# Kernel optimization log

Measured on AMD Instinct MI355X. Metric: run time of the kernel, lower is better.

The kernel has to match this reference:

```python
import jax, jax.numpy as jnp
import numpy as np

CLS_NUM = 2
SCALE = 8.0
NO_OBJ_SCALE = 1.0
EPS = 1e-7


def setup_inputs() -> dict:
    key = jax.random.key(0)
    k1, k2, k3, k4, k5, k6 = jax.random.split(key, 6)
    B, C, H, W, N = 8, CLS_NUM, 512, 512, 160
    predict = jax.random.normal(k1, (B, C, H, W), dtype=jnp.float32)
    b = jax.random.randint(k2, (N,), 0, B).astype(jnp.float32)
    c = jax.random.randint(k3, (N,), 0, C).astype(jnp.float32)
    cxy = jax.random.uniform(k4, (N, 2), minval=0.0, maxval=H * SCALE)
    wh = jax.random.uniform(k5, (N, 2), minval=64.0, maxval=256.0)
    ang = jax.random.uniform(k6, (N, 1), minval=-np.pi, maxval=np.pi)
    targets = jnp.concatenate([b[:, None], c[:, None], cxy, wh, ang], axis=1).astype(jnp.float32)
    return {"predict": predict, "targets": targets}


def _forward(predict, targets):
    B, C, H, W = predict.shape
    pred = jnp.transpose(predict, (0, 2, 3, 1))          # [B,H,W,C]
    conf_all = jax.nn.sigmoid(pred)
    heatmap = jnp.max(conf_all, axis=-1)                 # [B,H,W]

    bid = targets[:, 0].astype(jnp.int32)                # [N] batch ids
    cid = targets[:, 1].astype(jnp.int32)                # [N] class ids
    cx = targets[:, 2] / SCALE
    cy = targets[:, 3] / SCALE
    w = targets[:, 4] / SCALE
    h = targets[:, 5] / SCALE
    ang = targets[:, 6]
    cos, sin = jnp.cos(ang), jnp.sin(ang)
    # rotate box center into the rotated frame (same math as render_map)
    x = cx * cos + cy * sin
    y = -cx * sin + cy * cos
    x3, x4 = x - h / 2, x + h / 2
    y3, y4 = y - w / 2, y + w / 2
    x1, x2 = x3 - 0.5, x4 + 0.5
    y1, y2 = y3 - 0.5, y4 + 0.5

    gx = jnp.arange(W, dtype=jnp.float32)[None, :] + 0.5  # [1,W] -> broadcasts to [H,W]
    gy = jnp.arange(H, dtype=jnp.float32)[:, None] + 0.5  # [H,1]
    vx = cos[:, None, None] * gx + sin[:, None, None] * gy   # [N,H,W]
    vy = -sin[:, None, None] * gx + cos[:, None, None] * gy  # [N,H,W]

    def box_mask(lo_x, hi_x, lo_y, hi_y):
        return ((lo_x[:, None, None] <= vx) & (vx <= hi_x[:, None, None]) &
                (lo_y[:, None, None] <= vy) & (vy <= hi_y[:, None, None]))

    inner = box_mask(x3, x4, y3, y4)  # obj region, [N,H,W]
    outer = box_mask(x1, x2, y1, y2)  # expanded region (clears noobj)

    loss = jnp.float32(0.0)
    for cls in range(CLS_NUM):
        sel = (cid == cls)[:, None, None]
        obj_cnt = jax.ops.segment_sum((inner & sel).astype(jnp.float32), bid, num_segments=B)
        out_cnt = jax.ops.segment_sum((outer & sel).astype(jnp.float32), bid, num_segments=B)
        obj_mask = obj_cnt > 0            # [B,H,W]
        noobj_mask = out_cnt <= 0         # starts at 1, zeroed inside any expanded box
        conf_c = jnp.clip(conf_all[..., cls], EPS, 1.0 - EPS)
        n_obj = jnp.sum(obj_mask)
        n_noobj = jnp.sum(noobj_mask)
        # BCE with target 1 on obj cells, target 0 on noobj cells (tconf == obj mask)
        loss_obj = -jnp.sum(jnp.where(obj_mask, jnp.log(conf_c), 0.0)) / jnp.maximum(n_obj, 1)
        loss_noobj = -jnp.sum(jnp.where(noobj_mask, jnp.log(1.0 - conf_c), 0.0)) / jnp.maximum(n_noobj, 1)
        loss = loss + jnp.where(n_obj > 0, loss_obj + NO_OBJ_SCALE * loss_noobj, 0.0)
    return loss, heatmap


def reference(predict, targets):
    return _forward(predict, targets)
```

## Files before the change

kernel.cpp:

```cpp
#include <hip/hip_runtime.h>
#include <math.h>

#define CLS 2
#define BATCH 8
#define HH 512
#define WW 512
#define EPSV 1e-7f
#define INV_SCALE 0.125f

#define TCAP 256
#define NB 512


__global__ __launch_bounds__(256) void heatmap_main(
    const float* __restrict__ predict, const float* __restrict__ targets,
    int nT, float* __restrict__ out, double* __restrict__ gsum,
    int* __restrict__ gcnt)
{
    __shared__ int s_cnt;
    __shared__ float s_cos[TCAP], s_sin[TCAP];
    __shared__ float s_x3[TCAP], s_x4[TCAP], s_y3[TCAP], s_y4[TCAP];
    __shared__ int   s_cid[TCAP];

    const int tid = threadIdx.x;
    const int blockPix = blockIdx.x * 256;
    const int b  = blockPix >> 18;
    const int i  = (blockPix >> 9) & (HH - 1);
    const int j0 = blockPix & (WW - 1);

    if (tid == 0) s_cnt = 0;
    __syncthreads();

    const float gy = (float)i + 0.5f;

    for (int t = tid; t < nT; t += 256) {
        const float* tp = targets + t * 7;
        const int tb = (int)tp[0];
        if (tb != b) continue;
        const float cx = tp[2] * INV_SCALE, cy = tp[3] * INV_SCALE;
        const float w_ = tp[4] * INV_SCALE, h_ = tp[5] * INV_SCALE;
        const float ang = tp[6];
        const float cs = cosf(ang), sn = sinf(ang);
        const float x = cx * cs + cy * sn;
        const float y = -cx * sn + cy * cs;
        const float x3 = x - 0.5f * h_, x4 = x + 0.5f * h_;
        const float y3 = y - 0.5f * w_, y4 = y + 0.5f * w_;

        const float gxl = (float)j0 + 0.5f, gxh = (float)j0 + 255.5f;
        const float a1 = cs * gxl + sn * gy, a2 = cs * gxh + sn * gy;
        const float vxlo = fminf(a1, a2), vxhi = fmaxf(a1, a2);
        const float b1 = -sn * gxl + cs * gy, b2 = -sn * gxh + cs * gy;
        const float vylo = fminf(b1, b2), vyhi = fmaxf(b1, b2);

        const float M = 0.51f;
        if (vxhi >= x3 - M && vxlo <= x4 + M && vyhi >= y3 - M && vylo <= y4 + M) {
            int slot = atomicAdd(&s_cnt, 1);
            s_cos[slot] = cs; s_sin[slot] = sn;
            s_x3[slot] = x3; s_x4[slot] = x4;
            s_y3[slot] = y3; s_y4[slot] = y4;
            s_cid[slot] = (int)tp[1];
        }
    }
    __syncthreads();
    const int cnt = s_cnt;

    const int j = j0 + tid;
    const float gx = (float)j + 0.5f;
    int objm = 0, outm = 0;
    for (int n = 0; n < cnt; ++n) {
        const float cs = s_cos[n], sn = s_sin[n];
        const float vx = cs * gx + sn * gy;
        const float vy = -sn * gx + cs * gy;
        const float x3 = s_x3[n], x4 = s_x4[n], y3 = s_y3[n], y4 = s_y4[n];
        const bool in_  = (x3 <= vx) & (vx <= x4) & (y3 <= vy) & (vy <= y4);
        const bool out_ = (x3 - 0.5f <= vx) & (vx <= x4 + 0.5f) &
                          (y3 - 0.5f <= vy) & (vy <= y4 + 0.5f);
        const int c = s_cid[n];
        objm |= ((int)in_) << c;
        outm |= ((int)out_) << c;
    }

    const int base = (b * CLS * HH + i) * WW + j;
    const float p0 = predict[base];
    const float p1 = predict[base + HH * WW];
    const float conf0 = __builtin_amdgcn_rcpf(1.0f + __expf(-p0));
    const float conf1 = __builtin_amdgcn_rcpf(1.0f + __expf(-p1));
    out[1 + (b * HH + i) * WW + j] = fmaxf(conf0, conf1);

    float so0 = 0.f, so1 = 0.f, sn0 = 0.f, sn1 = 0.f;
    int co0 = 0, co1 = 0, cn0 = 0, cn1 = 0;
    {
        const float cc0 = fminf(fmaxf(conf0, EPSV), 1.0f - EPSV);
        const float cc1 = fminf(fmaxf(conf1, EPSV), 1.0f - EPSV);
        if (objm & 1) { so0 = __logf(cc0); co0 = 1; }
        if (objm & 2) { so1 = __logf(cc1); co1 = 1; }
        if (!(outm & 1)) { sn0 = __logf(1.0f - cc0); cn0 = 1; }
        if (!(outm & 2)) { sn1 = __logf(1.0f - cc1); cn1 = 1; }
    }

    #pragma unroll
    for (int off = 32; off >= 1; off >>= 1) {
        so0 += __shfl_down(so0, off); so1 += __shfl_down(so1, off);
        sn0 += __shfl_down(sn0, off); sn1 += __shfl_down(sn1, off);
        co0 += __shfl_down(co0, off); co1 += __shfl_down(co1, off);
        cn0 += __shfl_down(cn0, off); cn1 += __shfl_down(cn1, off);
    }

    __shared__ float r_f[4][4];
    __shared__ int   r_i[4][4];
    const int wv = tid >> 6, ln = tid & 63;
    if (ln == 0) {
        r_f[wv][0] = so0; r_f[wv][1] = so1; r_f[wv][2] = sn0; r_f[wv][3] = sn1;
        r_i[wv][0] = co0; r_i[wv][1] = co1; r_i[wv][2] = cn0; r_i[wv][3] = cn1;
    }
    __syncthreads();
    if (tid == 0) {
        const int bkt = blockIdx.x & (NB - 1);
        const float f0 = r_f[0][0] + r_f[1][0] + r_f[2][0] + r_f[3][0];
        const float f1 = r_f[0][1] + r_f[1][1] + r_f[2][1] + r_f[3][1];
        const float f2 = r_f[0][2] + r_f[1][2] + r_f[2][2] + r_f[3][2];
        const float f3 = r_f[0][3] + r_f[1][3] + r_f[2][3] + r_f[3][3];
        const int i0 = r_i[0][0] + r_i[1][0] + r_i[2][0] + r_i[3][0];
        const int i1 = r_i[0][1] + r_i[1][1] + r_i[2][1] + r_i[3][1];
        const int i2 = r_i[0][2] + r_i[1][2] + r_i[2][2] + r_i[3][2];
        const int i3 = r_i[0][3] + r_i[1][3] + r_i[2][3] + r_i[3][3];
        if (f0 != 0.f) atomicAdd(&gsum[0 * NB + bkt], (double)f0);
        if (f1 != 0.f) atomicAdd(&gsum[1 * NB + bkt], (double)f1);
        atomicAdd(&gsum[2 * NB + bkt], (double)f2);
        atomicAdd(&gsum[3 * NB + bkt], (double)f3);
        if (i0) atomicAdd(&gcnt[0 * NB + bkt], i0);
        if (i1) atomicAdd(&gcnt[1 * NB + bkt], i1);
        atomicAdd(&gcnt[2 * NB + bkt], i2);
        atomicAdd(&gcnt[3 * NB + bkt], i3);
    }
}

__global__ __launch_bounds__(512) void heatmap_finalize(
    const double* __restrict__ gsum, const int* __restrict__ gcnt,
    float* __restrict__ out)
{
    const int t = threadIdx.x;
    double f[4]; int c[4];
    #pragma unroll
    for (int q = 0; q < 4; ++q) { f[q] = gsum[q * NB + t]; c[q] = gcnt[q * NB + t]; }

    #pragma unroll
    for (int off = 32; off >= 1; off >>= 1) {
        #pragma unroll
        for (int q = 0; q < 4; ++q) {
            f[q] += __shfl_down(f[q], off);
            c[q] += __shfl_down(c[q], off);
        }
    }

    __shared__ double sf[8][4];
    __shared__ int    si[8][4];
    const int wv = t >> 6, ln = t & 63;
    if (ln == 0) {
        #pragma unroll
        for (int q = 0; q < 4; ++q) { sf[wv][q] = f[q]; si[wv][q] = c[q]; }
    }
    __syncthreads();
    if (t == 0) {
        double F[4] = {0, 0, 0, 0}; int C[4] = {0, 0, 0, 0};
        for (int w = 0; w < 8; ++w)
            #pragma unroll
            for (int q = 0; q < 4; ++q) { F[q] += sf[w][q]; C[q] += si[w][q]; }
        float loss = 0.0f;
        #pragma unroll
        for (int cls = 0; cls < CLS; ++cls) {
            const int no = C[cls];
            const int nn = C[2 + cls];
            if (no > 0) {
                const float lo  = -(float)F[cls]     / (float)(no > 1 ? no : 1);
                const float ln_ = -(float)F[2 + cls] / (float)(nn > 1 ? nn : 1);
                loss += lo + ln_;
            }
        }
        out[0] = loss;
    }
}

extern "C" void kernel_launch(void* const* d_in, const int* in_sizes, int n_in,
                              void* d_out, int out_size, void* d_ws, size_t ws_size,
                              hipStream_t stream) {
    const float* predict = (const float*)d_in[0];
    const float* targets = (const float*)d_in[1];
    const int nT = in_sizes[1] / 7;
    float* out = (float*)d_out;
    double* gsum = (double*)d_ws;
    int* gcnt = (int*)((char*)d_ws + 4 * NB * sizeof(double));

    hipMemsetAsync(d_ws, 0, 4 * NB * (sizeof(double) + sizeof(int)), stream);

    const int pixels = BATCH * HH * WW;
    heatmap_main<<<pixels / 256, 256, 0, stream>>>(predict, targets, nT, out,
                                                   gsum, gcnt);
    heatmap_finalize<<<1, 512, 0, stream>>>(gsum, gcnt, out);
}
```

Baseline: 94.93 us.

## Process two rows per block and fuse finalize via last-block reduction

New measurement: 135.9 us. 1.43x slower.

```diff
diff --git a/kernel.cpp b/kernel.cpp
--- a/kernel.cpp
+++ b/kernel.cpp
@@ -8,14 +8,17 @@
 #define EPSV 1e-7f
 #define INV_SCALE 0.125f
 
-#define TCAP 256
+#define TCAP 64
 #define NB 512
-
+#define PXB 1024
+#define NBLK (BATCH * HH * WW / PXB)
+
+#define WS_ZERO_BYTES 24840
 
 __global__ __launch_bounds__(256) void heatmap_main(
     const float* __restrict__ predict, const float* __restrict__ targets,
     int nT, float* __restrict__ out, double* __restrict__ gsum,
-    int* __restrict__ gcnt)
+    int* __restrict__ gcnt, int* __restrict__ leaf, int* __restrict__ root)
 {
     __shared__ int s_cnt;
     __shared__ float s_cos[TCAP], s_sin[TCAP];
@@ -23,34 +26,30 @@
     __shared__ int   s_cid[TCAP];
 
     const int tid = threadIdx.x;
-    const int blockPix = blockIdx.x * 256;
+    const int blockPix = blockIdx.x * PXB;
     const int b  = blockPix >> 18;
-    const int i  = (blockPix >> 9) & (HH - 1);
-    const int j0 = blockPix & (WW - 1);
+    const int r0 = (blockPix >> 9) & (HH - 1);
 
     if (tid == 0) s_cnt = 0;
     __syncthreads();
 
-    const float gy = (float)i + 0.5f;
-
+    const float gyl = (float)r0 + 0.5f, gyh = (float)r0 + 1.5f;
     for (int t = tid; t < nT; t += 256) {
         const float* tp = targets + t * 7;
-        const int tb = (int)tp[0];
-        if (tb != b) continue;
+        if ((int)tp[0] != b) continue;
         const float cx = tp[2] * INV_SCALE, cy = tp[3] * INV_SCALE;
         const float w_ = tp[4] * INV_SCALE, h_ = tp[5] * INV_SCALE;
-        const float ang = tp[6];
-        const float cs = cosf(ang), sn = sinf(ang);
+        const float cs = cosf(tp[6]), sn = sinf(tp[6]);
         const float x = cx * cs + cy * sn;
         const float y = -cx * sn + cy * cs;
         const float x3 = x - 0.5f * h_, x4 = x + 0.5f * h_;
         const float y3 = y - 0.5f * w_, y4 = y + 0.5f * w_;
 
-        const float gxl = (float)j0 + 0.5f, gxh = (float)j0 + 255.5f;
-        const float a1 = cs * gxl + sn * gy, a2 = cs * gxh + sn * gy;
-        const float vxlo = fminf(a1, a2), vxhi = fmaxf(a1, a2);
-        const float b1 = -sn * gxl + cs * gy, b2 = -sn * gxh + cs * gy;
-        const float vylo = fminf(b1, b2), vyhi = fmaxf(b1, b2);
+        const float gxl = 0.5f, gxh = 511.5f;
+        const float vxlo = fminf(cs * gxl, cs * gxh) + fminf(sn * gyl, sn * gyh);
+        const float vxhi = fmaxf(cs * gxl, cs * gxh) + fmaxf(sn * gyl, sn * gyh);
+        const float vylo = fminf(-sn * gxl, -sn * gxh) + fminf(cs * gyl, cs * gyh);
+        const float vyhi = fmaxf(-sn * gxl, -sn * gxh) + fmaxf(cs * gyl, cs * gyh);
 
         const float M = 0.51f;
         if (vxhi >= x3 - M && vxlo <= x4 + M && vyhi >= y3 - M && vylo <= y4 + M) {
@@ -64,38 +63,45 @@
     __syncthreads();
     const int cnt = s_cnt;
 
-    const int j = j0 + tid;
-    const float gx = (float)j + 0.5f;
-    int objm = 0, outm = 0;
-    for (int n = 0; n < cnt; ++n) {
-        const float cs = s_cos[n], sn = s_sin[n];
-        const float vx = cs * gx + sn * gy;
-        const float vy = -sn * gx + cs * gy;
-        const float x3 = s_x3[n], x4 = s_x4[n], y3 = s_y3[n], y4 = s_y4[n];
-        const bool in_  = (x3 <= vx) & (vx <= x4) & (y3 <= vy) & (vy <= y4);
-        const bool out_ = (x3 - 0.5f <= vx) & (vx <= x4 + 0.5f) &
-                          (y3 - 0.5f <= vy) & (vy <= y4 + 0.5f);
-        const int c = s_cid[n];
-        objm |= ((int)in_) << c;
-        outm |= ((int)out_) << c;
-    }
-
-    const int base = (b * CLS * HH + i) * WW + j;
-    const float p0 = predict[base];
-    const float p1 = predict[base + HH * WW];
-    const float conf0 = __builtin_amdgcn_rcpf(1.0f + __expf(-p0));
-    const float conf1 = __builtin_amdgcn_rcpf(1.0f + __expf(-p1));
-    out[1 + (b * HH + i) * WW + j] = fmaxf(conf0, conf1);
-
     float so0 = 0.f, so1 = 0.f, sn0 = 0.f, sn1 = 0.f;
     int co0 = 0, co1 = 0, cn0 = 0, cn1 = 0;
-    {
+
+    #pragma unroll
+    for (int k = 0; k < 4; ++k) {
+        const int off = tid + 256 * k;
+        const int ro  = off >> 9;
+        const int col = off & (WW - 1);
+        const int row = r0 + ro;
+        const float gx = (float)col + 0.5f;
+        const float gy = (float)row + 0.5f;
+
+        int objm = 0, outm = 0;
+        for (int n = 0; n < cnt; ++n) {
+            const float cs = s_cos[n], sn = s_sin[n];
+            const float vx = cs * gx + sn * gy;
+            const float vy = -sn * gx + cs * gy;
+            const float x3 = s_x3[n], x4 = s_x4[n], y3 = s_y3[n], y4 = s_y4[n];
+            const bool in_  = (x3 <= vx) & (vx <= x4) & (y3 <= vy) & (vy <= y4);
+            const bool out_ = (x3 - 0.5f <= vx) & (vx <= x4 + 0.5f) &
+                              (y3 - 0.5f <= vy) & (vy <= y4 + 0.5f);
+            const int c = s_cid[n];
+            objm |= ((int)in_) << c;
+            outm |= ((int)out_) << c;
+        }
+
+        const int base = ((b * CLS) * HH + row) * WW + col;
+        const float p0 = predict[base];
+        const float p1 = predict[base + HH * WW];
+        const float conf0 = __builtin_amdgcn_rcpf(1.0f + __expf(-p0));
+        const float conf1 = __builtin_amdgcn_rcpf(1.0f + __expf(-p1));
+        out[1 + (b * HH + row) * WW + col] = fmaxf(conf0, conf1);
+
         const float cc0 = fminf(fmaxf(conf0, EPSV), 1.0f - EPSV);
         const float cc1 = fminf(fmaxf(conf1, EPSV), 1.0f - EPSV);
-        if (objm & 1) { so0 = __logf(cc0); co0 = 1; }
-        if (objm & 2) { so1 = __logf(cc1); co1 = 1; }
-        if (!(outm & 1)) { sn0 = __logf(1.0f - cc0); cn0 = 1; }
-        if (!(outm & 2)) { sn1 = __logf(1.0f - cc1); cn1 = 1; }
+        if (objm & 1) { so0 += __logf(cc0); co0 += 1; }
+        if (objm & 2) { so1 += __logf(cc1); co1 += 1; }
+        if (!(outm & 1)) { sn0 += __logf(1.0f - cc0); cn0 += 1; }
+        if (!(outm & 2)) { sn1 += __logf(1.0f - cc1); cn1 += 1; }
     }
 
     #pragma unroll
@@ -114,70 +120,75 @@
         r_i[wv][0] = co0; r_i[wv][1] = co1; r_i[wv][2] = cn0; r_i[wv][3] = cn1;
     }
     __syncthreads();
+
+    __shared__ int s_isLast;
     if (tid == 0) {
         const int bkt = blockIdx.x & (NB - 1);
-        const float f0 = r_f[0][0] + r_f[1][0] + r_f[2][0] + r_f[3][0];
-        const float f1 = r_f[0][1] + r_f[1][1] + r_f[2][1] + r_f[3][1];
-        const float f2 = r_f[0][2] + r_f[1][2] + r_f[2][2] + r_f[3][2];
-        const float f3 = r_f[0][3] + r_f[1][3] + r_f[2][3] + r_f[3][3];
-        const int i0 = r_i[0][0] + r_i[1][0] + r_i[2][0] + r_i[3][0];
-        const int i1 = r_i[0][1] + r_i[1][1] + r_i[2][1] + r_i[3][1];
-        const int i2 = r_i[0][2] + r_i[1][2] + r_i[2][2] + r_i[3][2];
-        const int i3 = r_i[0][3] + r_i[1][3] + r_i[2][3] + r_i[3][3];
-        if (f0 != 0.f) atomicAdd(&gsum[0 * NB + bkt], (double)f0);
-        if (f1 != 0.f) atomicAdd(&gsum[1 * NB + bkt], (double)f1);
-        atomicAdd(&gsum[2 * NB + bkt], (double)f2);
-        atomicAdd(&gsum[3 * NB + bkt], (double)f3);
-        if (i0) atomicAdd(&gcnt[0 * NB + bkt], i0);
-        if (i1) atomicAdd(&gcnt[1 * NB + bkt], i1);
-        atomicAdd(&gcnt[2 * NB + bkt], i2);
-        atomicAdd(&gcnt[3 * NB + bkt], i3);
-    }
-}
-
-__global__ __launch_bounds__(512) void heatmap_finalize(
-    const double* __restrict__ gsum, const int* __restrict__ gcnt,
-    float* __restrict__ out)
-{
-    const int t = threadIdx.x;
-    double f[4]; int c[4];
-    #pragma unroll
-    for (int q = 0; q < 4; ++q) { f[q] = gsum[q * NB + t]; c[q] = gcnt[q * NB + t]; }
-
-    #pragma unroll
-    for (int off = 32; off >= 1; off >>= 1) {
+        float f[4]; int c[4];
         #pragma unroll
         for (int q = 0; q < 4; ++q) {
-            f[q] += __shfl_down(f[q], off);
-            c[q] += __shfl_down(c[q], off);
-        }
-    }
-
-    __shared__ double sf[8][4];
-    __shared__ int    si[8][4];
-    const int wv = t >> 6, ln = t & 63;
-    if (ln == 0) {
+            f[q] = r_f[0][q] + r_f[1][q] + r_f[2][q] + r_f[3][q];
+            c[q] = r_i[0][q] + r_i[1][q] + r_i[2][q] + r_i[3][q];
+        }
         #pragma unroll
-        for (int q = 0; q < 4; ++q) { sf[wv][q] = f[q]; si[wv][q] = c[q]; }
-    }
-    __syncthreads();
-    if (t == 0) {
-        double F[4] = {0, 0, 0, 0}; int C[4] = {0, 0, 0, 0};
-        for (int w = 0; w < 8; ++w)
-            #pragma unroll
-            for (int q = 0; q < 4; ++q) { F[q] += sf[w][q]; C[q] += si[w][q]; }
-        float loss = 0.0f;
+        for (int q = 0; q < 4; ++q) {
+            if (f[q] != 0.f) atomicAdd(&gsum[q * NB + bkt], (double)f[q]);
+            if (c[q])        atomicAdd(&gcnt[q * NB + bkt], c[q]);
+        }
+        __threadfence();
+        int isLast = 0;
+        const int lo = atomicAdd(&leaf[blockIdx.x & 63], 1);
+        if (lo == (NBLK / 64) - 1) {
+            const int ro_ = atomicAdd(root, 1);
+            if (ro_ == 63) isLast = 1;
+        }
+        s_isLast = isLast;
+    }
+    __syncthreads();
+
+    if (s_isLast) {
+        double f[4] = {0, 0, 0, 0}; long long c[4] = {0, 0, 0, 0};
+        for (int t = tid; t < NB; t += 256) {
+            #pragma unroll
+            for (int q = 0; q < 4; ++q) {
+                f[q] += atomicAdd(&gsum[q * NB + t], 0.0);
+                c[q] += atomicAdd(&gcnt[q * NB + t], 0);
+            }
+        }
         #pragma unroll
-        for (int cls = 0; cls < CLS; ++cls) {
-            const int no = C[cls];
-            const int nn = C[2 + cls];
-            if (no > 0) {
-                const float lo  = -(float)F[cls]     / (float)(no > 1 ? no : 1);
-                const float ln_ = -(float)F[2 + cls] / (float)(nn > 1 ? nn : 1);
-                loss += lo + ln_;
-            }
-        }
-        out[0] = loss;
+        for (int off = 32; off >= 1; off >>= 1) {
+            #pragma unroll
+            for (int q = 0; q < 4; ++q) {
+                f[q] += __shfl_down(f[q], off);
+                c[q] += __shfl_down(c[q], off);
+            }
+        }
+        __shared__ double zf[4][4];
+        __shared__ long long zi[4][4];
+        if (ln == 0) {
+            #pragma unroll
+            for (int q = 0; q < 4; ++q) { zf[wv][q] = f[q]; zi[wv][q] = c[q]; }
+        }
+        __syncthreads();
+        if (tid == 0) {
+            double F[4]; long long C[4];
+            #pragma unroll
+            for (int q = 0; q < 4; ++q) {
+                F[q] = zf[0][q] + zf[1][q] + zf[2][q] + zf[3][q];
+                C[q] = zi[0][q] + zi[1][q] + zi[2][q] + zi[3][q];
+            }
+            float loss = 0.0f;
+            #pragma unroll
+            for (int cls = 0; cls < CLS; ++cls) {
+                const long long no = C[cls], nn = C[2 + cls];
+                if (no > 0) {
+                    const float lo  = -(float)F[cls]     / (float)(no > 1 ? no : 1);
+                    const float ln_ = -(float)F[2 + cls] / (float)(nn > 1 ? nn : 1);
+                    loss += lo + ln_;
+                }
+            }
+            out[0] = loss;
+        }
     }
 }
 
@@ -188,13 +199,13 @@
     const float* targets = (const float*)d_in[1];
     const int nT = in_sizes[1] / 7;
     float* out = (float*)d_out;
-    double* gsum = (double*)d_ws;
-    int* gcnt = (int*)((char*)d_ws + 4 * NB * sizeof(double));
-
-    hipMemsetAsync(d_ws, 0, 4 * NB * (sizeof(double) + sizeof(int)), stream);
-
-    const int pixels = BATCH * HH * WW;
-    heatmap_main<<<pixels / 256, 256, 0, stream>>>(predict, targets, nT, out,
-                                                   gsum, gcnt);
-    heatmap_finalize<<<1, 512, 0, stream>>>(gsum, gcnt, out);
+    char* ws = (char*)d_ws;
+    double* gsum = (double*)ws;
+    int* gcnt = (int*)(ws + 16384);
+    int* leaf = (int*)(ws + 24576);
+    int* root = (int*)(ws + 24832);
+
+    hipMemsetAsync(d_ws, 0, WS_ZERO_BYTES, stream);
+    heatmap_main<<<NBLK, 256, 0, stream>>>(predict, targets, nT, out,
+                                           gsum, gcnt, leaf, root);
 }
```

## Precompute target geometry in prep kernel and simplify log-sigmoid loss math

Applied to the files above, without the earlier changes.

Result: faster. 89.68 us (-5.5%).

```diff
diff --git a/kernel.cpp b/kernel.cpp
--- a/kernel.cpp
+++ b/kernel.cpp
@@ -5,15 +5,40 @@
 #define BATCH 8
 #define HH 512
 #define WW 512
-#define EPSV 1e-7f
 #define INV_SCALE 0.125f
-
-#define TCAP 256
+#define LOGEPS -16.118095651f
+
+#define TCAP 160
 #define NB 512
-
+#define TSTR 256
+
+
+__global__ __launch_bounds__(512) void heatmap_prep(
+    const float* __restrict__ targets, int nT,
+    float* __restrict__ tprep, double* __restrict__ gsum, int* __restrict__ gcnt)
+{
+    const int t = threadIdx.x;
+    for (int q = t; q < 4 * NB; q += 512) { gsum[q] = 0.0; gcnt[q] = 0; }
+    if (t < nT) {
+        const float* tp = targets + t * 7;
+        const float cs = cosf(tp[6]), sn = sinf(tp[6]);
+        const float cx = tp[2] * INV_SCALE, cy = tp[3] * INV_SCALE;
+        const float w_ = tp[4] * INV_SCALE, h_ = tp[5] * INV_SCALE;
+        const float x = cx * cs + cy * sn;
+        const float y = -cx * sn + cy * cs;
+        ((int*)tprep)[0 * TSTR + t] = (int)tp[0];
+        ((int*)tprep)[1 * TSTR + t] = (int)tp[1];
+        tprep[2 * TSTR + t] = cs;
+        tprep[3 * TSTR + t] = sn;
+        tprep[4 * TSTR + t] = x - 0.5f * h_;
+        tprep[5 * TSTR + t] = x + 0.5f * h_;
+        tprep[6 * TSTR + t] = y - 0.5f * w_;
+        tprep[7 * TSTR + t] = y + 0.5f * w_;
+    }
+}
 
 __global__ __launch_bounds__(256) void heatmap_main(
-    const float* __restrict__ predict, const float* __restrict__ targets,
+    const float* __restrict__ predict, const float* __restrict__ tprep,
     int nT, float* __restrict__ out, double* __restrict__ gsum,
     int* __restrict__ gcnt)
 {
@@ -33,18 +58,10 @@
 
     const float gy = (float)i + 0.5f;
 
-    for (int t = tid; t < nT; t += 256) {
-        const float* tp = targets + t * 7;
-        const int tb = (int)tp[0];
-        if (tb != b) continue;
-        const float cx = tp[2] * INV_SCALE, cy = tp[3] * INV_SCALE;
-        const float w_ = tp[4] * INV_SCALE, h_ = tp[5] * INV_SCALE;
-        const float ang = tp[6];
-        const float cs = cosf(ang), sn = sinf(ang);
-        const float x = cx * cs + cy * sn;
-        const float y = -cx * sn + cy * cs;
-        const float x3 = x - 0.5f * h_, x4 = x + 0.5f * h_;
-        const float y3 = y - 0.5f * w_, y4 = y + 0.5f * w_;
+    if (tid < nT && ((const int*)tprep)[tid] == b) {
+        const float cs = tprep[2 * TSTR + tid], sn = tprep[3 * TSTR + tid];
+        const float x3 = tprep[4 * TSTR + tid], x4 = tprep[5 * TSTR + tid];
+        const float y3 = tprep[6 * TSTR + tid], y4 = tprep[7 * TSTR + tid];
 
         const float gxl = (float)j0 + 0.5f, gxh = (float)j0 + 255.5f;
         const float a1 = cs * gxl + sn * gy, a2 = cs * gxh + sn * gy;
@@ -58,7 +75,7 @@
             s_cos[slot] = cs; s_sin[slot] = sn;
             s_x3[slot] = x3; s_x4[slot] = x4;
             s_y3[slot] = y3; s_y4[slot] = y4;
-            s_cid[slot] = (int)tp[1];
+            s_cid[slot] = ((const int*)tprep)[TSTR + tid];
         }
     }
     __syncthreads();
@@ -83,27 +100,32 @@
     const int base = (b * CLS * HH + i) * WW + j;
     const float p0 = predict[base];
     const float p1 = predict[base + HH * WW];
-    const float conf0 = __builtin_amdgcn_rcpf(1.0f + __expf(-p0));
-    const float conf1 = __builtin_amdgcn_rcpf(1.0f + __expf(-p1));
-    out[1 + (b * HH + i) * WW + j] = fmaxf(conf0, conf1);
-
-    float so0 = 0.f, so1 = 0.f, sn0 = 0.f, sn1 = 0.f;
-    int co0 = 0, co1 = 0, cn0 = 0, cn1 = 0;
-    {
-        const float cc0 = fminf(fmaxf(conf0, EPSV), 1.0f - EPSV);
-        const float cc1 = fminf(fmaxf(conf1, EPSV), 1.0f - EPSV);
-        if (objm & 1) { so0 = __logf(cc0); co0 = 1; }
-        if (objm & 2) { so1 = __logf(cc1); co1 = 1; }
-        if (!(outm & 1)) { sn0 = __logf(1.0f - cc0); cn0 = 1; }
-        if (!(outm & 2)) { sn1 = __logf(1.0f - cc1); cn1 = 1; }
-    }
+    const float t0 = __expf(p0), t1 = __expf(p1);
+    const float s0 = 1.0f + t0,  s1 = 1.0f + t1;
+    const float c0 = t0 * __builtin_amdgcn_rcpf(s0);
+    const float c1 = t1 * __builtin_amdgcn_rcpf(s1);
+    float l10 = -__logf(s0);
+    float l11 = -__logf(s1);
+    const float lc0 = fmaxf(p0 + l10, LOGEPS);
+    const float lc1 = fmaxf(p1 + l11, LOGEPS);
+    l10 = fmaxf(l10, LOGEPS);
+    l11 = fmaxf(l11, LOGEPS);
+
+    out[1 + (b * HH + i) * WW + j] = fmaxf(c0, c1);
+
+    float so0 = (objm & 1) ? lc0 : 0.0f;
+    float so1 = (objm & 2) ? lc1 : 0.0f;
+    float sn0 = (outm & 1) ? 0.0f : l10;
+    float sn1 = (outm & 2) ? 0.0f : l11;
+    const int co0 = (int)__popcll(__ballot(objm & 1));
+    const int co1 = (int)__popcll(__ballot(objm & 2));
+    const int cn0 = (int)__popcll(__ballot(!(outm & 1)));
+    const int cn1 = (int)__popcll(__ballot(!(outm & 2)));
 
     #pragma unroll
     for (int off = 32; off >= 1; off >>= 1) {
         so0 += __shfl_down(so0, off); so1 += __shfl_down(so1, off);
         sn0 += __shfl_down(sn0, off); sn1 += __shfl_down(sn1, off);
-        co0 += __shfl_down(co0, off); co1 += __shfl_down(co1, off);
-        cn0 += __shfl_down(cn0, off); cn1 += __shfl_down(cn1, off);
     }
 
     __shared__ float r_f[4][4];
@@ -116,22 +138,13 @@
     __syncthreads();
     if (tid == 0) {
         const int bkt = blockIdx.x & (NB - 1);
-        const float f0 = r_f[0][0] + r_f[1][0] + r_f[2][0] + r_f[3][0];
-        const float f1 = r_f[0][1] + r_f[1][1] + r_f[2][1] + r_f[3][1];
-        const float f2 = r_f[0][2] + r_f[1][2] + r_f[2][2] + r_f[3][2];
-        const float f3 = r_f[0][3] + r_f[1][3] + r_f[2][3] + r_f[3][3];
-        const int i0 = r_i[0][0] + r_i[1][0] + r_i[2][0] + r_i[3][0];
-        const int i1 = r_i[0][1] + r_i[1][1] + r_i[2][1] + r_i[3][1];
-        const int i2 = r_i[0][2] + r_i[1][2] + r_i[2][2] + r_i[3][2];
-        const int i3 = r_i[0][3] + r_i[1][3] + r_i[2][3] + r_i[3][3];
-        if (f0 != 0.f) atomicAdd(&gsum[0 * NB + bkt], (double)f0);
-        if (f1 != 0.f) atomicAdd(&gsum[1 * NB + bkt], (double)f1);
-        atomicAdd(&gsum[2 * NB + bkt], (double)f2);
-        atomicAdd(&gsum[3 * NB + bkt], (double)f3);
-        if (i0) atomicAdd(&gcnt[0 * NB + bkt], i0);
-        if (i1) atomicAdd(&gcnt[1 * NB + bkt], i1);
-        atomicAdd(&gcnt[2 * NB + bkt], i2);
-        atomicAdd(&gcnt[3 * NB + bkt], i3);
+        #pragma unroll
+        for (int q = 0; q < 4; ++q) {
+            const float f = r_f[0][q] + r_f[1][q] + r_f[2][q] + r_f[3][q];
+            const int   c = r_i[0][q] + r_i[1][q] + r_i[2][q] + r_i[3][q];
+            if (f != 0.0f) atomicAdd(&gsum[q * NB + bkt], (double)f);
+            if (c)         atomicAdd(&gcnt[q * NB + bkt], c);
+        }
     }
 }
 
@@ -188,13 +201,14 @@
     const float* targets = (const float*)d_in[1];
     const int nT = in_sizes[1] / 7;
     float* out = (float*)d_out;
-    double* gsum = (double*)d_ws;
-    int* gcnt = (int*)((char*)d_ws + 4 * NB * sizeof(double));
-
-    hipMemsetAsync(d_ws, 0, 4 * NB * (sizeof(double) + sizeof(int)), stream);
-
+    char* ws = (char*)d_ws;
+    double* gsum = (double*)ws;
+    int* gcnt = (int*)(ws + 16384);
+    float* tprep = (float*)(ws + 24576);
+
+    heatmap_prep<<<1, 512, 0, stream>>>(targets, nT, tprep, gsum, gcnt);
     const int pixels = BATCH * HH * WW;
-    heatmap_main<<<pixels / 256, 256, 0, stream>>>(predict, targets, nT, out,
+    heatmap_main<<<pixels / 256, 256, 0, stream>>>(predict, tprep, nT, out,
                                                    gsum, gcnt);
     heatmap_finalize<<<1, 512, 0, stream>>>(gsum, gcnt, out);
 }
```
